# Optimization experiments

Measured on AMD Instinct MI355X. Metric: run time of the kernel, lower is better.

## Reference

```python
import jax, jax.numpy as jnp
import numpy as np

B, Q, K, D = 16, 2048, 2048, 128
NEG = -1000000.0  # matches torch module's mask fill value (not -inf)


def setup_inputs() -> dict:
    key = jax.random.key(0)
    kq, kk, kv, kl = jax.random.split(key, 4)
    q = jax.random.normal(kq, (B, Q, D), dtype=jnp.float32)
    k = jax.random.normal(kk, (B, K, D), dtype=jnp.float32)
    v = jax.random.normal(kv, (B, K, D), dtype=jnp.float32)
    valid_lens = jax.random.randint(kl, (B, 1), 0, K, dtype=jnp.int32)
    return {"q": q, "k": k, "v": v, "valid_lens": valid_lens}


def reference(q, k, v, valid_lens):
    d = q.shape[-1]
    # scores: (B, Q, K)
    weight = jnp.einsum('bqd,bkd->bqk', q, k) / jnp.sqrt(jnp.asarray(d, q.dtype))
    # mask: key position j valid iff j < valid_len[b]; broadcast over query dim
    mask = jnp.arange(k.shape[1])[None, None, :] < valid_lens[:, :, None]  # (B,1,K)
    weight = jnp.where(mask, weight, NEG)
    score = jax.nn.softmax(weight, axis=-1)
    return jnp.einsum('bqk,bkv->bqv', score, v)
```

## Files before the change

### kernel.cpp

```cpp
#include <hip/hip_runtime.h>

constexpr int NB = 16;
constexpr int NQ = 2048;
constexpr int NK = 2048;
constexpr int ND = 128;
constexpr int KVBLK = 64;
constexpr int NTILE = NK / KVBLK;
constexpr int TILE_USH = KVBLK * ND;
constexpr float SCALE2 = 0.12751744751442557f;

typedef __attribute__((ext_vector_type(4))) float f4;
typedef __attribute__((ext_vector_type(16))) float f32x16;
typedef __attribute__((ext_vector_type(8))) unsigned short us8;
typedef __attribute__((ext_vector_type(8))) __bf16 bf16x8;
typedef __attribute__((ext_vector_type(4))) unsigned int u32x4;

static __device__ __forceinline__ unsigned short f2bf(float f) {
    unsigned u = __builtin_bit_cast(unsigned, f);
    u += 0x7fffu + ((u >> 16) & 1u);
    return (unsigned short)(u >> 16);
}
static __device__ __forceinline__ f4 splat4(float x) { f4 r = {x,x,x,x}; return r; }

static __device__ __forceinline__ float fexp2(float x) {
    float r;
    asm("v_exp_f32 %0, %1" : "=v"(r) : "v"(x));
    return r;
}

static __device__ __forceinline__ void load_lds16(const unsigned short* g, unsigned short* l) {
    __builtin_amdgcn_global_load_lds(
        (const __attribute__((address_space(1))) void*)g,
        (__attribute__((address_space(3))) void*)l,
        16, 0, 0);
}

static __device__ __forceinline__ unsigned cvt_pk_bf16(float lo, float hi) {
    unsigned r;
    asm("v_cvt_pk_bf16_f32 %0, %1, %2" : "=v"(r) : "v"(lo), "v"(hi));
    return r;
}

__global__ __launch_bounds__(256)
void prep_kv5(const float* __restrict__ kg, const float* __restrict__ vg,
              const int* __restrict__ vlen,
              unsigned short* __restrict__ wk, unsigned short* __restrict__ wvt)
{
    const int b   = blockIdx.y;
    const int t   = blockIdx.x;
    const int kv0 = t * KVBLK;

    {
        const int v = vlen[b];
        const int Leff = (v <= 0) ? NK : v;
        if (kv0 >= Leff) return;
    }

    const int t0  = threadIdx.x;

    __shared__ __align__(16) unsigned short vl[64 * 136];

    {
        const int kv = t0 >> 2;
        const int c  = t0 & 3;
        const float* gp = kg + (size_t)(b * NK + kv0 + kv) * ND + c * 32;
        unsigned short* ob = wk + (size_t)(b * NTILE + t) * TILE_USH;
        #pragma unroll
        for (int g = 0; g < 4; ++g) {
            f4 f0 = *(const f4*)(gp + g * 8);
            f4 f1 = *(const f4*)(gp + g * 8 + 4);
            us8 w;
            #pragma unroll
            for (int i = 0; i < 4; ++i) { w[i] = f2bf(f0[i]); w[i+4] = f2bf(f1[i]); }
            const int d0 = c * 32 + g * 8;
            const int f  = (kv >> 5) * 8 + (d0 >> 4);
            const int off = f * 512 + ((d0 >> 3) & 1) * 256 + (kv & 31) * 8;
            *(us8*)(ob + off) = w;
        }
    }
    {
        const int kv = t0 >> 2;
        const int d0 = (t0 & 3) * 32;
        const float* gp = vg + (size_t)(b * NK + kv0 + kv) * ND + d0;
        unsigned short* lb = &vl[kv * 136 + d0];
        #pragma unroll
        for (int g = 0; g < 4; ++g) {
            f4 f0 = *(const f4*)(gp + g * 8);
            f4 f1 = *(const f4*)(gp + g * 8 + 4);
            us8 w;
            #pragma unroll
            for (int i = 0; i < 4; ++i) { w[i] = f2bf(f0[i]); w[i+4] = f2bf(f1[i]); }
            *(us8*)(lb + g * 8) = w;
        }
    }
    __syncthreads();
    {
        unsigned short* ob = wvt + (size_t)(b * NTILE + t) * TILE_USH;
        #pragma unroll
        for (int iter = 0; iter < 4; ++iter) {
            const int cid = iter * 256 + t0;
            const int f   = cid >> 6;
            const int l   = cid & 63;
            const int kb  = (f >> 2) * 16 + (l >> 5) * 8;
            const int d   = (f & 3) * 32 + (l & 31);
            us8 w;
            #pragma unroll
            for (int j = 0; j < 8; ++j) w[j] = vl[(kb + j) * 136 + d];
            *(us8*)(ob + cid * 8) = w;
        }
    }
}

__global__ __launch_bounds__(128, 2)
void attn_fused19(const float* __restrict__ qg, const int* __restrict__ vlen,
                  const unsigned short* __restrict__ wk,
                  const unsigned short* __restrict__ wvt,
                  float* __restrict__ og)
{
    const int bid     = blockIdx.x;
    const int quarter = bid >> 8;
    const int j       = bid & 255;
    const int slot    = j & 7;
    const int rank    = (quarter & 1) ? (15 - slot) : slot;
    const int qc      = (j >> 3) + ((quarter >> 1) << 5);
    const int q0      = qc * 32;

    int b = 0;
    {
        int Ls[16];
        #pragma unroll
        for (int i = 0; i < 16; ++i) {
            const int v = vlen[i];
            Ls[i] = (v <= 0) ? NK : v;
        }
        #pragma unroll
        for (int bb = 0; bb < 16; ++bb) {
            int r = 0;
            #pragma unroll
            for (int cc = 0; cc < 16; ++cc)
                r += (Ls[cc] > Ls[bb] || (Ls[cc] == Ls[bb] && cc < bb)) ? 1 : 0;
            if (r == rank) b = bb;
        }
    }

    const int tid  = threadIdx.x;
    const int grp  = tid >> 6;
    const int lane = tid & 63;
    const int lq   = lane & 31;
    const int hi   = lane >> 5;

    const int L = vlen[b];
    const bool uniform = (L <= 0);
    const int Leff = uniform ? NK : L;
    const int ntiles = (Leff + KVBLK - 1) / KVBLK;
    const int ng = (ntiles > grp) ? ((ntiles - grp + 1) >> 1) : 0;

    __shared__ __align__(16) float accb[32 * 128];
    __shared__ float mlb[64];

    bf16x8 aq[8];
    {
        const float* qp = qg + (size_t)(b * NQ + q0 + lq) * ND + hi * 8;
        #pragma unroll
        for (int c = 0; c < 8; ++c) {
            f4 f0 = *(const f4*)(qp + c * 16);
            f4 f1 = *(const f4*)(qp + c * 16 + 4);
            us8 u;
            #pragma unroll
            for (int i = 0; i < 4; ++i) {
                u[i]     = f2bf(f0[i] * SCALE2);
                u[i + 4] = f2bf(f1[i] * SCALE2);
            }
            aq[c] = __builtin_bit_cast(bf16x8, u);
        }
    }

    const unsigned short* kbg = wk  + (size_t)b * NTILE * TILE_USH;
    const unsigned short* vbg = wvt + (size_t)b * NTILE * TILE_USH;

    float m_r = -1e30f;
    float l_r = 0.f;
    f32x16 accO[4];
    #pragma unroll
    for (int dc = 0; dc < 4; ++dc)
        #pragma unroll
        for (int r = 0; r < 16; ++r) accO[dc][r] = 0.f;

    for (int i = 0; i < ng; ++i) {
        const int tile = 2 * i + grp;
        const int kv0  = tile * KVBLK;

        us8 kf[16];
        {
            const unsigned short* ksrc = kbg + (size_t)tile * TILE_USH + lane * 8;
            #pragma unroll
            for (int c = 0; c < 16; ++c)
                kf[c] = *(const us8*)(ksrc + c * 512);
        }
        f32x16 sA, sB;
        #pragma unroll
        for (int r = 0; r < 16; ++r) { sA[r] = 0.f; sB[r] = 0.f; }
        #pragma unroll
        for (int c = 0; c < 8; ++c) {
            sA = __builtin_amdgcn_mfma_f32_32x32x16_bf16(
                __builtin_bit_cast(bf16x8, kf[c]), aq[c], sA, 0, 0, 0);
            sB = __builtin_amdgcn_mfma_f32_32x32x16_bf16(
                __builtin_bit_cast(bf16x8, kf[8 + c]), aq[c], sB, 0, 0, 0);
        }
        __builtin_amdgcn_sched_barrier(0);

        us8 vf[16];
        {
            const unsigned short* vsrc = vbg + (size_t)tile * TILE_USH + lane * 8;
            #pragma unroll
            for (int f = 0; f < 16; ++f)
                vf[f] = *(const us8*)(vsrc + f * 512);
        }

        if (uniform) {
            #pragma unroll
            for (int r = 0; r < 16; ++r) { sA[r] = 0.f; sB[r] = 0.f; }
        } else {
            const int lim0 = L - kv0 - 4 * hi;
            const int lim1 = lim0 - 32;
            #pragma unroll
            for (int r = 0; r < 16; ++r) {
                const int rc = (r & 3) + 8 * (r >> 2);
                sA[r] = (rc >= lim0) ? -__builtin_inff() : sA[r];
                sB[r] = (rc >= lim1) ? -__builtin_inff() : sB[r];
            }
        }

        float tt[11];
        #pragma unroll
        for (int g3 = 0; g3 < 5; ++g3)
            tt[g3] = fmaxf(fmaxf(sA[3 * g3], sA[3 * g3 + 1]), sA[3 * g3 + 2]);
        tt[5] = fmaxf(fmaxf(sA[15], sB[0]), sB[1]);
        #pragma unroll
        for (int g3 = 0; g3 < 4; ++g3)
            tt[6 + g3] = fmaxf(fmaxf(sB[3 * g3 + 2], sB[3 * g3 + 3]), sB[3 * g3 + 4]);
        tt[10] = fmaxf(sB[14], sB[15]);
        const float u0 = fmaxf(fmaxf(tt[0], tt[1]), tt[2]);
        const float u1 = fmaxf(fmaxf(tt[3], tt[4]), tt[5]);
        const float u2 = fmaxf(fmaxf(tt[6], tt[7]), tt[8]);
        const float u3 = fmaxf(tt[9], tt[10]);
        const float pm = fmaxf(fmaxf(u0, u1), fmaxf(u2, u3));
        float pmax = fmaxf(pm, __shfl_xor(pm, 32));

        if (__any(pmax > m_r)) {
            const float mnew = fmaxf(m_r, pmax);
            const float sc = fexp2(m_r - mnew);
            m_r = mnew;
            l_r *= sc;
            #pragma unroll
            for (int r = 0; r < 16; ++r) {
                const int src = ((r & 3) + 8 * (r >> 2) + 4 * hi) + (lane & 32);
                const float scr = __shfl(sc, src);
                accO[0][r] *= scr; accO[1][r] *= scr;
                accO[2][r] *= scr; accO[3][r] *= scr;
            }
        }

        float p0[16], p1[16];
        #pragma unroll
        for (int r = 0; r < 16; ++r) {
            p0[r] = fexp2(sA[r] - m_r);
            p1[r] = fexp2(sB[r] - m_r);
        }
        float sm[8];
        #pragma unroll
        for (int i2 = 0; i2 < 8; ++i2)
            sm[i2] = (p0[i2] + p0[i2 + 8]) + (p1[i2] + p1[i2 + 8]);
        #pragma unroll
        for (int i2 = 0; i2 < 4; ++i2) sm[i2] += sm[i2 + 4];
        float rsum = (sm[0] + sm[1]) + (sm[2] + sm[3]);
        rsum += __shfl_xor(rsum, 32);
        l_r += rsum;

        unsigned cw[16];
        #pragma unroll
        for (int i2 = 0; i2 < 8; ++i2) cw[i2] = cvt_pk_bf16(p0[2 * i2], p0[2 * i2 + 1]);
        #pragma unroll
        for (int i2 = 0; i2 < 8; ++i2) cw[8 + i2] = cvt_pk_bf16(p1[2 * i2], p1[2 * i2 + 1]);

        bf16x8 pa[4];
        #pragma unroll
        for (int ks = 0; ks < 4; ++ks) {
            const int a = 4 * ks;
            const unsigned u = hi ? cw[a]     : cw[a + 2];
            const unsigned v = hi ? cw[a + 1] : cw[a + 3];
            const unsigned up = __shfl_xor((int)u, 32);
            const unsigned vp = __shfl_xor((int)v, 32);
            u32x4 w;
            w[0] = hi ? up        : cw[a];
            w[1] = hi ? vp        : cw[a + 1];
            w[2] = hi ? cw[a + 2] : up;
            w[3] = hi ? cw[a + 3] : vp;
            pa[ks] = __builtin_bit_cast(bf16x8, w);
        }

        #pragma unroll
        for (int dc = 0; dc < 4; ++dc) {
            #pragma unroll
            for (int ks = 0; ks < 4; ++ks) {
                accO[dc] = __builtin_amdgcn_mfma_f32_32x32x16_bf16(
                    pa[ks], __builtin_bit_cast(bf16x8, vf[ks * 4 + dc]), accO[dc], 0, 0, 0);
            }
        }
    }

    if (grp == 1) {
        #pragma unroll
        for (int dc = 0; dc < 4; ++dc) {
            #pragma unroll
            for (int q4 = 0; q4 < 4; ++q4) {
                f4 v;
                #pragma unroll
                for (int c = 0; c < 4; ++c) v[c] = accO[dc][q4 * 4 + c];
                *(f4*)&accb[(((dc * 4 + q4) * 64) + lane) * 4] = v;
            }
        }
        if (hi == 0) {
            mlb[lq]      = m_r;
            mlb[32 + lq] = l_r;
        }
    }
    __syncthreads();
    if (grp == 0) {
        const float m1 = mlb[lq];
        const float l1 = mlb[32 + lq];
        const float m  = fmaxf(m_r, m1);
        const float a0 = fexp2(m_r - m), a1 = fexp2(m1 - m);
        const float linv = 1.0f / (a0 * l_r + a1 * l1);
        const float s0v = a0 * linv, s1v = a1 * linv;
        float* ob = og + (size_t)(b * NQ + q0) * ND;
        #pragma unroll
        for (int dc = 0; dc < 4; ++dc) {
            #pragma unroll
            for (int q4 = 0; q4 < 4; ++q4) {
                f4 o1 = *(const f4*)&accb[(((dc * 4 + q4) * 64) + lane) * 4];
                #pragma unroll
                for (int c = 0; c < 4; ++c) {
                    const int r = q4 * 4 + c;
                    const int row = c + 8 * q4 + 4 * hi;
                    const float s0r = __shfl(s0v, row + (lane & 32));
                    const float s1r = __shfl(s1v, row + (lane & 32));
                    ob[(size_t)row * ND + dc * 32 + lq] = accO[dc][r] * s0r + o1[c] * s1r;
                }
            }
        }
    }
}

__global__ __launch_bounds__(256, 2)
void attn_fused(const float* __restrict__ qg, const float* __restrict__ kg,
                const float* __restrict__ vg, const int* __restrict__ vlen,
                float* __restrict__ og)
{
    const int b    = blockIdx.y;
    const int q0   = blockIdx.x * 64;
    const int tid  = threadIdx.x;
    const int wid  = tid >> 6;
    const int lane = tid & 63;
    const int lrow = lane & 15;
    const int lgrp = lane >> 4;
    constexpr float SCALE = 0.08838834764831844f;

    const int L = vlen[b];
    const bool uniform = (L <= 0);
    const int Leff = uniform ? NK : L;
    const int nt32 = (Leff + 31) / 32;

    __shared__ __align__(16) unsigned short kt[32 * 136];
    __shared__ __align__(16) unsigned short vt[128 * 40];
    __shared__ __align__(16) float pt[4][16 * 36];

    bf16x8 aqf[4];
    {
        const float* qp = qg + (size_t)(b * NQ + q0 + wid * 16 + lrow) * ND + lgrp * 8;
        #pragma unroll
        for (int c = 0; c < 4; ++c) {
            f4 f0 = *(const f4*)(qp + c * 32);
            f4 f1 = *(const f4*)(qp + c * 32 + 4);
            us8 u;
            #pragma unroll
            for (int i = 0; i < 4; ++i) {
                u[i]     = f2bf(f0[i] * SCALE);
                u[i + 4] = f2bf(f1[i] * SCALE);
            }
            aqf[c] = __builtin_bit_cast(bf16x8, u);
        }
    }

    float m_r[4], l_r[4];
    f4 accO[8];
    #pragma unroll
    for (int r = 0; r < 4; ++r) { m_r[r] = -__builtin_inff(); l_r[r] = 0.f; }
    #pragma unroll
    for (int dc = 0; dc < 8; ++dc) accO[dc] = splat4(0.f);

    for (int t = 0; t < nt32; ++t) {
        const int kv0 = t * 32;
        __syncthreads();
        {
            const int r  = tid >> 3;
            const int c0 = (tid & 7) * 16;
            const float* gp = kg + (size_t)(b * NK + kv0 + r) * ND + c0;
            f4 f0 = *(const f4*)(gp);
            f4 f1 = *(const f4*)(gp + 4);
            f4 f2 = *(const f4*)(gp + 8);
            f4 f3 = *(const f4*)(gp + 12);
            us8 w0, w1;
            #pragma unroll
            for (int i = 0; i < 4; ++i) {
                w0[i]     = f2bf(f0[i]);
                w0[i + 4] = f2bf(f1[i]);
                w1[i]     = f2bf(f2[i]);
                w1[i + 4] = f2bf(f3[i]);
            }
            unsigned short* dst = &kt[r * 136 + c0];
            *(us8*)(dst)     = w0;
            *(us8*)(dst + 8) = w1;
        }
        {
            const int d  = tid & 127;
            const int g2 = tid >> 7;
            const float* gp = vg + (size_t)(b * NK + kv0 + g2 * 16) * ND + d;
            us8 w0, w1;
            #pragma unroll
            for (int jj = 0; jj < 8; ++jj) {
                w0[jj] = f2bf(gp[(size_t)jj * ND]);
                w1[jj] = f2bf(gp[(size_t)(jj + 8) * ND]);
            }
            unsigned short* dst = &vt[d * 40 + g2 * 16];
            *(us8*)(dst)     = w0;
            *(us8*)(dst + 8) = w1;
        }
        __syncthreads();

        f4 s0 = splat4(0.f), s1 = splat4(0.f);
        #pragma unroll
        for (int c = 0; c < 4; ++c) {
            bf16x8 bk0 = __builtin_bit_cast(bf16x8,
                *(const us8*)&kt[lrow * 136 + c * 32 + lgrp * 8]);
            s0 = __builtin_amdgcn_mfma_f32_16x16x32_bf16(aqf[c], bk0, s0, 0, 0, 0);
            bf16x8 bk1 = __builtin_bit_cast(bf16x8,
                *(const us8*)&kt[(16 + lrow) * 136 + c * 32 + lgrp * 8]);
            s1 = __builtin_amdgcn_mfma_f32_16x16x32_bf16(aqf[c], bk1, s1, 0, 0, 0);
        }

        const int col0 = kv0 + lrow;
        if (uniform) {
            s0 = splat4(0.f);
            s1 = splat4(0.f);
        } else {
            if (col0 >= L)      s0 = splat4(-__builtin_inff());
            if (col0 + 16 >= L) s1 = splat4(-__builtin_inff());
        }

        float pm[4];
        #pragma unroll
        for (int r = 0; r < 4; ++r) pm[r] = fmaxf(s0[r], s1[r]);
        #pragma unroll
        for (int off = 8; off > 0; off >>= 1) {
            #pragma unroll
            for (int r = 0; r < 4; ++r)
                pm[r] = fmaxf(pm[r], __shfl_xor(pm[r], off));
        }
        float pr0[4], pr1[4], rs[4], sc[4];
        #pragma unroll
        for (int r = 0; r < 4; ++r) {
            float mn = fmaxf(m_r[r], pm[r]);
            sc[r]  = __expf(m_r[r] - mn);
            m_r[r] = mn;
            pr0[r] = __expf(s0[r] - mn);
            pr1[r] = __expf(s1[r] - mn);
            rs[r]  = pr0[r] + pr1[r];
        }
        #pragma unroll
        for (int off = 8; off > 0; off >>= 1) {
            #pragma unroll
            for (int r = 0; r < 4; ++r)
                rs[r] += __shfl_xor(rs[r], off);
        }
        #pragma unroll
        for (int r = 0; r < 4; ++r) l_r[r] = l_r[r] * sc[r] + rs[r];
        #pragma unroll
        for (int dc = 0; dc < 8; ++dc) {
            #pragma unroll
            for (int r = 0; r < 4; ++r) accO[dc][r] *= sc[r];
        }

        float* pw = pt[wid];
        #pragma unroll
        for (int r = 0; r < 4; ++r) {
            pw[(lgrp * 4 + r) * 36 + lrow]      = pr0[r];
            pw[(lgrp * 4 + r) * 36 + 16 + lrow] = pr1[r];
        }
        asm volatile("s_waitcnt lgkmcnt(0)" ::: "memory");
        f4 a0 = *(const f4*)&pw[lrow * 36 + lgrp * 8];
        f4 a1 = *(const f4*)&pw[lrow * 36 + lgrp * 8 + 4];
        us8 au;
        #pragma unroll
        for (int i = 0; i < 4; ++i) { au[i] = f2bf(a0[i]); au[i + 4] = f2bf(a1[i]); }
        bf16x8 ap = __builtin_bit_cast(bf16x8, au);

        #pragma unroll
        for (int dc = 0; dc < 8; ++dc) {
            bf16x8 bv = __builtin_bit_cast(bf16x8,
                *(const us8*)&vt[(dc * 16 + lrow) * 40 + lgrp * 8]);
            accO[dc] = __builtin_amdgcn_mfma_f32_16x16x32_bf16(ap, bv, accO[dc], 0, 0, 0);
        }
    }

    float inv[4];
    #pragma unroll
    for (int r = 0; r < 4; ++r) inv[r] = 1.0f / l_r[r];
    float* op = og + (size_t)(b * NQ + q0 + wid * 16) * ND;
    #pragma unroll
    for (int dc = 0; dc < 8; ++dc) {
        #pragma unroll
        for (int r = 0; r < 4; ++r)
            op[(lgrp * 4 + r) * ND + dc * 16 + lrow] = accO[dc][r] * inv[r];
    }
}

extern "C" void kernel_launch(void* const* d_in, const int* in_sizes, int n_in,
                              void* d_out, int out_size, void* d_ws, size_t ws_size,
                              hipStream_t stream) {
    (void)in_sizes; (void)n_in; (void)out_size;
    const float* q  = (const float*)d_in[0];
    const float* k  = (const float*)d_in[1];
    const float* v  = (const float*)d_in[2];
    const int*   vl = (const int*)d_in[3];
    float* out = (float*)d_out;

    const size_t kvbytes = 2 * (size_t)NB * NK * ND * sizeof(unsigned short);
    if (ws_size >= kvbytes) {
        unsigned short* wk  = (unsigned short*)d_ws;
        unsigned short* wvt = wk + (size_t)NB * NK * ND;
        hipLaunchKernelGGL(prep_kv5, dim3(NTILE, NB), dim3(256), 0, stream, k, v, vl, wk, wvt);
        hipLaunchKernelGGL(attn_fused19, dim3((NQ / 32) * NB), dim3(128), 0, stream,
                           q, vl, wk, wvt, out);
    } else {
        hipLaunchKernelGGL(attn_fused, dim3(NQ / 64, NB), dim3(256), 0, stream,
                           q, k, v, vl, out);
    }
}
```

Measured before the change: 51.94 us.

## Split KV loop across three waves using 32-key subtiles per wave

The attention kernel now runs three waves per block instead of two. Each wave processes interleaved 32-key subtiles instead of 64-key tiles, and the partial results of waves 1 and 2 are merged by wave 0 through two LDS buffers. This is meant to raise wave-level parallelism and latency hiding while halving per-wave register use for K/V fragments. In exchange it issues smaller MFMA batches per iteration, needs more LDS, and adds a two-stage softmax merge at the end.

Result: slower. 69.09 us (+33.0%).

```diff
diff --git a/kernel.cpp b/kernel.cpp
--- a/kernel.cpp
+++ b/kernel.cpp
@@ -28,13 +28,6 @@
     return r;
 }
 
-static __device__ __forceinline__ void load_lds16(const unsigned short* g, unsigned short* l) {
-    __builtin_amdgcn_global_load_lds(
-        (const __attribute__((address_space(1))) void*)g,
-        (__attribute__((address_space(3))) void*)l,
-        16, 0, 0);
-}
-
 static __device__ __forceinline__ unsigned cvt_pk_bf16(float lo, float hi) {
     unsigned r;
     asm("v_cvt_pk_bf16_f32 %0, %1, %2" : "=v"(r) : "v"(lo), "v"(hi));
@@ -111,8 +104,8 @@
     }
 }
 
-__global__ __launch_bounds__(128, 2)
-void attn_fused19(const float* __restrict__ qg, const int* __restrict__ vlen,
+__global__ __launch_bounds__(192, 3)
+void attn_fused20(const float* __restrict__ qg, const int* __restrict__ vlen,
                   const unsigned short* __restrict__ wk,
                   const unsigned short* __restrict__ wvt,
                   float* __restrict__ og)
@@ -152,11 +145,11 @@
     const int L = vlen[b];
     const bool uniform = (L <= 0);
     const int Leff = uniform ? NK : L;
-    const int ntiles = (Leff + KVBLK - 1) / KVBLK;
-    const int ng = (ntiles > grp) ? ((ntiles - grp + 1) >> 1) : 0;
-
-    __shared__ __align__(16) float accb[32 * 128];
-    __shared__ float mlb[64];
+    const int nsub = (Leff + 31) >> 5;
+    const int ng = (nsub > grp) ? ((nsub - grp + 2) / 3) : 0;
+
+    __shared__ __align__(16) float accb[2][32 * 128];
+    __shared__ float mlb[2][64];
 
     bf16x8 aq[8];
     {
@@ -187,64 +180,53 @@
         for (int r = 0; r < 16; ++r) accO[dc][r] = 0.f;
 
     for (int i = 0; i < ng; ++i) {
-        const int tile = 2 * i + grp;
-        const int kv0  = tile * KVBLK;
-
-        us8 kf[16];
+        const int s   = 3 * i + grp;
+        const int kv0 = s * 32;
+        const size_t soff = (size_t)(s >> 1) * TILE_USH + (s & 1) * 4096;
+
+        us8 kf[8];
         {
-            const unsigned short* ksrc = kbg + (size_t)tile * TILE_USH + lane * 8;
-            #pragma unroll
-            for (int c = 0; c < 16; ++c)
+            const unsigned short* ksrc = kbg + soff + lane * 8;
+            #pragma unroll
+            for (int c = 0; c < 8; ++c)
                 kf[c] = *(const us8*)(ksrc + c * 512);
         }
-        f32x16 sA, sB;
-        #pragma unroll
-        for (int r = 0; r < 16; ++r) { sA[r] = 0.f; sB[r] = 0.f; }
-        #pragma unroll
-        for (int c = 0; c < 8; ++c) {
+        f32x16 sA;
+        #pragma unroll
+        for (int r = 0; r < 16; ++r) sA[r] = 0.f;
+        #pragma unroll
+        for (int c = 0; c < 8; ++c)
             sA = __builtin_amdgcn_mfma_f32_32x32x16_bf16(
                 __builtin_bit_cast(bf16x8, kf[c]), aq[c], sA, 0, 0, 0);
-            sB = __builtin_amdgcn_mfma_f32_32x32x16_bf16(
-                __builtin_bit_cast(bf16x8, kf[8 + c]), aq[c], sB, 0, 0, 0);
-        }
         __builtin_amdgcn_sched_barrier(0);
 
-        us8 vf[16];
+        us8 vf[8];
         {
-            const unsigned short* vsrc = vbg + (size_t)tile * TILE_USH + lane * 8;
-            #pragma unroll
-            for (int f = 0; f < 16; ++f)
+            const unsigned short* vsrc = vbg + soff + lane * 8;
+            #pragma unroll
+            for (int f = 0; f < 8; ++f)
                 vf[f] = *(const us8*)(vsrc + f * 512);
         }
 
         if (uniform) {
             #pragma unroll
-            for (int r = 0; r < 16; ++r) { sA[r] = 0.f; sB[r] = 0.f; }
+            for (int r = 0; r < 16; ++r) sA[r] = 0.f;
         } else {
             const int lim0 = L - kv0 - 4 * hi;
-            const int lim1 = lim0 - 32;
             #pragma unroll
             for (int r = 0; r < 16; ++r) {
                 const int rc = (r & 3) + 8 * (r >> 2);
                 sA[r] = (rc >= lim0) ? -__builtin_inff() : sA[r];
-                sB[r] = (rc >= lim1) ? -__builtin_inff() : sB[r];
-            }
-        }
-
-        float tt[11];
-        #pragma unroll
-        for (int g3 = 0; g3 < 5; ++g3)
-            tt[g3] = fmaxf(fmaxf(sA[3 * g3], sA[3 * g3 + 1]), sA[3 * g3 + 2]);
-        tt[5] = fmaxf(fmaxf(sA[15], sB[0]), sB[1]);
-        #pragma unroll
-        for (int g3 = 0; g3 < 4; ++g3)
-            tt[6 + g3] = fmaxf(fmaxf(sB[3 * g3 + 2], sB[3 * g3 + 3]), sB[3 * g3 + 4]);
-        tt[10] = fmaxf(sB[14], sB[15]);
-        const float u0 = fmaxf(fmaxf(tt[0], tt[1]), tt[2]);
-        const float u1 = fmaxf(fmaxf(tt[3], tt[4]), tt[5]);
-        const float u2 = fmaxf(fmaxf(tt[6], tt[7]), tt[8]);
-        const float u3 = fmaxf(tt[9], tt[10]);
-        const float pm = fmaxf(fmaxf(u0, u1), fmaxf(u2, u3));
+            }
+        }
+
+        float t0 = fmaxf(fmaxf(sA[0], sA[1]), sA[2]);
+        float t1 = fmaxf(fmaxf(sA[3], sA[4]), sA[5]);
+        float t2 = fmaxf(fmaxf(sA[6], sA[7]), sA[8]);
+        float t3 = fmaxf(fmaxf(sA[9], sA[10]), sA[11]);
+        float t4 = fmaxf(fmaxf(sA[12], sA[13]), sA[14]);
+        const float pm = fmaxf(fmaxf(fmaxf(t0, t1), fmaxf(t2, t3)),
+                               fmaxf(t4, sA[15]));
         float pmax = fmaxf(pm, __shfl_xor(pm, 32));
 
         if (__any(pmax > m_r)) {
@@ -261,31 +243,25 @@
             }
         }
 
-        float p0[16], p1[16];
-        #pragma unroll
-        for (int r = 0; r < 16; ++r) {
-            p0[r] = fexp2(sA[r] - m_r);
-            p1[r] = fexp2(sB[r] - m_r);
-        }
+        float p0[16];
+        #pragma unroll
+        for (int r = 0; r < 16; ++r) p0[r] = fexp2(sA[r] - m_r);
         float sm[8];
         #pragma unroll
-        for (int i2 = 0; i2 < 8; ++i2)
-            sm[i2] = (p0[i2] + p0[i2 + 8]) + (p1[i2] + p1[i2 + 8]);
+        for (int i2 = 0; i2 < 8; ++i2) sm[i2] = p0[i2] + p0[i2 + 8];
         #pragma unroll
         for (int i2 = 0; i2 < 4; ++i2) sm[i2] += sm[i2 + 4];
         float rsum = (sm[0] + sm[1]) + (sm[2] + sm[3]);
         rsum += __shfl_xor(rsum, 32);
         l_r += rsum;
 
-        unsigned cw[16];
+        unsigned cw[8];
         #pragma unroll
         for (int i2 = 0; i2 < 8; ++i2) cw[i2] = cvt_pk_bf16(p0[2 * i2], p0[2 * i2 + 1]);
-        #pragma unroll
-        for (int i2 = 0; i2 < 8; ++i2) cw[8 + i2] = cvt_pk_bf16(p1[2 * i2], p1[2 * i2 + 1]);
-
-        bf16x8 pa[4];
-        #pragma unroll
-        for (int ks = 0; ks < 4; ++ks) {
+
+        bf16x8 pa[2];
+        #pragma unroll
+        for (int ks = 0; ks < 2; ++ks) {
             const int a = 4 * ks;
             const unsigned u = hi ? cw[a]     : cw[a + 2];
             const unsigned v = hi ? cw[a + 1] : cw[a + 3];
@@ -302,14 +278,15 @@
         #pragma unroll
         for (int dc = 0; dc < 4; ++dc) {
             #pragma unroll
-            for (int ks = 0; ks < 4; ++ks) {
+            for (int ks = 0; ks < 2; ++ks) {
                 accO[dc] = __builtin_amdgcn_mfma_f32_32x32x16_bf16(
                     pa[ks], __builtin_bit_cast(bf16x8, vf[ks * 4 + dc]), accO[dc], 0, 0, 0);
             }
         }
     }
 
-    if (grp == 1) {
+    if (grp >= 1) {
+        float* ab = accb[grp - 1];
         #pragma unroll
         for (int dc = 0; dc < 4; ++dc) {
             #pragma unroll
@@ -317,36 +294,55 @@
                 f4 v;
                 #pragma unroll
                 for (int c = 0; c < 4; ++c) v[c] = accO[dc][q4 * 4 + c];
-                *(f4*)&accb[(((dc * 4 + q4) * 64) + lane) * 4] = v;
+                *(f4*)&ab[(((dc * 4 + q4) * 64) + lane) * 4] = v;
             }
         }
         if (hi == 0) {
-            mlb[lq]      = m_r;
-            mlb[32 + lq] = l_r;
+            mlb[grp - 1][lq]      = m_r;
+            mlb[grp - 1][32 + lq] = l_r;
         }
     }
     __syncthreads();
     if (grp == 0) {
-        const float m1 = mlb[lq];
-        const float l1 = mlb[32 + lq];
-        const float m  = fmaxf(m_r, m1);
-        const float a0 = fexp2(m_r - m), a1 = fexp2(m1 - m);
-        const float linv = 1.0f / (a0 * l_r + a1 * l1);
-        const float s0v = a0 * linv, s1v = a1 * linv;
+        #pragma unroll
+        for (int g = 0; g < 2; ++g) {
+            const float mg = mlb[g][lq];
+            const float lg = mlb[g][32 + lq];
+            const float mn = fmaxf(m_r, mg);
+            const float a0 = fexp2(m_r - mn);
+            const float a1 = fexp2(mg - mn);
+            m_r = mn;
+            l_r = a0 * l_r + a1 * lg;
+            float a0v[16], a1v[16];
+            #pragma unroll
+            for (int r = 0; r < 16; ++r) {
+                const int row = (r & 3) + 8 * (r >> 2) + 4 * hi;
+                a0v[r] = __shfl(a0, row + (lane & 32));
+                a1v[r] = __shfl(a1, row + (lane & 32));
+            }
+            const float* ab = accb[g];
+            #pragma unroll
+            for (int dc = 0; dc < 4; ++dc) {
+                #pragma unroll
+                for (int q4 = 0; q4 < 4; ++q4) {
+                    f4 o1 = *(const f4*)&ab[(((dc * 4 + q4) * 64) + lane) * 4];
+                    #pragma unroll
+                    for (int c = 0; c < 4; ++c) {
+                        const int r = q4 * 4 + c;
+                        accO[dc][r] = accO[dc][r] * a0v[r] + o1[c] * a1v[r];
+                    }
+                }
+            }
+        }
+        const float inv = 1.0f / l_r;
         float* ob = og + (size_t)(b * NQ + q0) * ND;
         #pragma unroll
         for (int dc = 0; dc < 4; ++dc) {
             #pragma unroll
-            for (int q4 = 0; q4 < 4; ++q4) {
-                f4 o1 = *(const f4*)&accb[(((dc * 4 + q4) * 64) + lane) * 4];
-                #pragma unroll
-                for (int c = 0; c < 4; ++c) {
-                    const int r = q4 * 4 + c;
-                    const int row = c + 8 * q4 + 4 * hi;
-                    const float s0r = __shfl(s0v, row + (lane & 32));
-                    const float s1r = __shfl(s1v, row + (lane & 32));
-                    ob[(size_t)row * ND + dc * 32 + lq] = accO[dc][r] * s0r + o1[c] * s1r;
-                }
+            for (int r = 0; r < 16; ++r) {
+                const int row = (r & 3) + 8 * (r >> 2) + 4 * hi;
+                const float invr = __shfl(inv, row + (lane & 32));
+                ob[(size_t)row * ND + dc * 32 + lq] = accO[dc][r] * invr;
             }
         }
     }
@@ -540,7 +536,7 @@
         unsigned short* wk  = (unsigned short*)d_ws;
         unsigned short* wvt = wk + (size_t)NB * NK * ND;
         hipLaunchKernelGGL(prep_kv5, dim3(NTILE, NB), dim3(256), 0, stream, k, v, vl, wk, wvt);
-        hipLaunchKernelGGL(attn_fused19, dim3((NQ / 32) * NB), dim3(128), 0, stream,
+        hipLaunchKernelGGL(attn_fused20, dim3((NQ / 32) * NB), dim3(192), 0, stream,
                            q, vl, wk, wvt, out);
     } else {
         hipLaunchKernelGGL(attn_fused, dim3(NQ / 64, NB), dim3(256), 0, stream,
```
